# Kernel optimization log

Measured on AMD Instinct MI355X. Metric: run time of the kernel, lower is better.

The kernel has to match this reference:

```python
import jax, jax.numpy as jnp
import numpy as np

TEMPERATURE = 1.0


def setup_inputs() -> dict:
    key = jax.random.key(0)
    k1, k2, k3 = jax.random.split(key, 3)
    B, N, D = 4, 4096, 128
    x = jax.random.normal(k1, (B, N, D), dtype=jnp.float32)
    # nn.Linear(dim, dim): weight [D, D], bias [D] (kaiming-uniform-ish scale)
    bound = 1.0 / np.sqrt(D)
    W = jax.random.uniform(k2, (D, D), dtype=jnp.float32, minval=-bound, maxval=bound)
    b = jax.random.uniform(k3, (D,), dtype=jnp.float32, minval=-bound, maxval=bound)
    return {"x": x, "W": W, "b": b}


def reference(x, W, b):
    # Linear projection (torch Linear: x @ W.T + b)
    h = jnp.einsum('bnd,ed->bne', x, W) + b            # [B, N, D]
    # Pairwise Euclidean distance via ||a||^2 + ||b||^2 - 2 a.b (avoids O(N^2*D) diff tensor)
    sq = jnp.sum(h * h, axis=-1)                        # [B, N]
    gram = jnp.einsum('bnd,bmd->bnm', h, h)             # [B, N, N]
    d2 = jnp.maximum(sq[:, :, None] + sq[:, None, :] - 2.0 * gram, 0.0)
    distances = jnp.sqrt(d2)                            # [B, N, N]
    return jnp.exp(-distances * TEMPERATURE)
```

## Files before the change

kernel.cpp:

```cpp
#include <hip/hip_runtime.h>


typedef float  f32x4   __attribute__((ext_vector_type(4)));
typedef float  f32x16  __attribute__((ext_vector_type(16)));
typedef short  bf16x8  __attribute__((ext_vector_type(8)));
typedef __attribute__((address_space(3))) void       lds_void_t;
typedef const __attribute__((address_space(1))) void gvoid_t;

__device__ inline float bf2f(unsigned int u) {
    union { unsigned int i; float f; } c; c.i = u << 16; return c.f;
}
__device__ inline unsigned short f2bf(float f) {
    union { float f; unsigned int i; } c; c.f = f;
    unsigned int r = c.i + 0x7fffu + ((c.i >> 16) & 1u);
    return (unsigned short)(r >> 16);
}

#define KA_ROWS 32
__global__ __launch_bounds__(256) void proj_kernel(
    const float* __restrict__ x, const float* __restrict__ W,
    const float* __restrict__ bias, unsigned short* __restrict__ h,
    float* __restrict__ sq)
{
    __shared__ __align__(16) unsigned short W5[32 * 4 * 32 * 4];
    __shared__ float xs[KA_ROWS][132];
    const int t = threadIdx.x;
    const long r0 = (long)blockIdx.x * KA_ROWS;

    for (int q = t; q < 4096; q += 256) {
        float4 w4 = ((const float4*)W)[q];
        int e = q >> 5, d4 = q & 31;
        int eb = e >> 2, ei = e & 3;
        ushort4 o;
        o.x = f2bf(w4.x); o.y = f2bf(w4.y); o.z = f2bf(w4.z); o.w = f2bf(w4.w);
        *(ushort4*)&W5[d4 * 256 + ei * 64 + ((eb ^ d4) & 31) * 4] = o;
    }
    const float4* xsrc = (const float4*)(x + r0 * 128);
    for (int q = t; q < KA_ROWS * 32; q += 256) {
        float4 v = xsrc[q];
        int r = q >> 5, d = (q & 31) << 2;
        xs[r][d] = v.x; xs[r][d + 1] = v.y; xs[r][d + 2] = v.z; xs[r][d + 3] = v.w;
    }
    __syncthreads();

    const int eb = t & 31, rb = t >> 5;
    const int e0 = eb * 4, rr0 = rb * 4;

    float acc_[4][4];
    #pragma unroll
    for (int ei = 0; ei < 4; ++ei) {
        float bv = bias[e0 + ei];
        #pragma unroll
        for (int ri = 0; ri < 4; ++ri) acc_[ri][ei] = bv;
    }

    for (int d4 = 0; d4 < 32; ++d4) {
        float wv[4][4];
        #pragma unroll
        for (int ei = 0; ei < 4; ++ei) {
            ushort4 u = *(const ushort4*)&W5[d4 * 256 + ei * 64 + ((eb ^ d4) & 31) * 4];
            wv[ei][0] = bf2f(u.x); wv[ei][1] = bf2f(u.y);
            wv[ei][2] = bf2f(u.z); wv[ei][3] = bf2f(u.w);
        }
        #pragma unroll
        for (int ri = 0; ri < 4; ++ri) {
            float4 xv = *(const float4*)&xs[rr0 + ri][d4 * 4];
            #pragma unroll
            for (int ei = 0; ei < 4; ++ei) {
                acc_[ri][ei] = fmaf(xv.x, wv[ei][0],
                               fmaf(xv.y, wv[ei][1],
                               fmaf(xv.z, wv[ei][2],
                               fmaf(xv.w, wv[ei][3], acc_[ri][ei]))));
            }
        }
    }

    float s[4] = {0.f, 0.f, 0.f, 0.f};
    #pragma unroll
    for (int ri = 0; ri < 4; ++ri) {
        ushort4 o;
        float v0 = bf2f(o.x = f2bf(acc_[ri][0]));
        float v1 = bf2f(o.y = f2bf(acc_[ri][1]));
        float v2 = bf2f(o.z = f2bf(acc_[ri][2]));
        float v3 = bf2f(o.w = f2bf(acc_[ri][3]));
        s[ri] = v0 * v0 + v1 * v1 + v2 * v2 + v3 * v3;
        *(ushort4*)&h[(r0 + rr0 + ri) * 128 + e0] = o;
    }
    #pragma unroll
    for (int ri = 0; ri < 4; ++ri) {
        #pragma unroll
        for (int m = 16; m > 0; m >>= 1) s[ri] += __shfl_xor(s[ri], m, 64);
    }
    if (eb == 0) {
        #pragma unroll
        for (int ri = 0; ri < 4; ++ri) sq[r0 + rr0 + ri] = s[ri];
    }
}

__global__ __launch_bounds__(512, 2) void gram_kernel(
    const unsigned short* __restrict__ h, const float* __restrict__ sq,
    float* __restrict__ out)
{
    __shared__ __align__(16) unsigned short hsI[256 * 128];
    __shared__ __align__(16) unsigned short hsJ[256 * 128];
    const int bid = blockIdx.x;
    const int xcd = bid & 7;
    const int bb  = xcd >> 1;
    const int tloc = ((bid >> 3) << 1) | (xcd & 1);
    const int it = tloc >> 4, jt = tloc & 15;
    const int i0 = bb * 4096 + it * 256;
    const int j0 = bb * 4096 + jt * 256;
    const int t = threadIdx.x, w = t >> 6, lane = t & 63;

    const char* hb = (const char*)h;
    #pragma unroll
    for (int q = 0; q < 8; ++q) {
        int p   = (q * 512 + t) << 4;
        int row = p >> 8;
        int c   = (p >> 4) & 15;
        int cs  = c ^ (row & 15);
        unsigned off = (unsigned)p;
        __builtin_amdgcn_global_load_lds(
            (gvoid_t*)(hb + ((long)(i0 + row) << 8) + (cs << 4)),
            (lds_void_t*)(((char*)hsI) + off), 16, 0, 0);
        __builtin_amdgcn_global_load_lds(
            (gvoid_t*)(hb + ((long)(j0 + row) << 8) + (cs << 4)),
            (lds_void_t*)(((char*)hsJ) + off), 16, 0, 0);
    }
    __syncthreads();

    const int wr = w >> 2, wc = w & 3;
    const int l31 = lane & 31, lh = lane >> 5;
    f32x16 acc[4][2] = {};
    const char* hI = (const char*)hsI;
    const char* hJ = (const char*)hsJ;

    #pragma unroll
    for (int ks = 0; ks < 8; ++ks) {
        bf16x8 af[4], bg[2];
        #pragma unroll
        for (int rb = 0; rb < 4; ++rb) {
            int rowA = wr * 128 + rb * 32 + l31;
            int cA = ((ks * 2 + lh) ^ (rowA & 15)) << 4;
            af[rb] = *(const bf16x8*)(hI + (rowA << 8) + cA);
        }
        #pragma unroll
        for (int nb = 0; nb < 2; ++nb) {
            int rowB = wc * 64 + nb * 32 + l31;
            int cB = ((ks * 2 + lh) ^ (rowB & 15)) << 4;
            bg[nb] = *(const bf16x8*)(hJ + (rowB << 8) + cB);
        }
        #pragma unroll
        for (int rb = 0; rb < 4; ++rb)
            #pragma unroll
            for (int nb = 0; nb < 2; ++nb)
                acc[rb][nb] = __builtin_amdgcn_mfma_f32_32x32x16_bf16(
                    af[rb], bg[nb], acc[rb][nb], 0, 0, 0);
    }

    float sqj_r[2];
    #pragma unroll
    for (int nb = 0; nb < 2; ++nb) sqj_r[nb] = sq[j0 + wc * 64 + nb * 32 + l31];

    #pragma unroll
    for (int rb = 0; rb < 4; ++rb) {
        #pragma unroll
        for (int reg = 0; reg < 16; ++reg) {
            int il = wr * 128 + rb * 32 + (reg & 3) + 8 * (reg >> 2) + 4 * lh;
            float sqi_v = sq[i0 + il];
            #pragma unroll
            for (int nb = 0; nb < 2; ++nb) {
                int jl = wc * 64 + nb * 32 + l31;
                float g  = acc[rb][nb][reg];
                float d2 = fmaxf(fmaf(g, -2.0f, sqi_v + sqj_r[nb]), 0.0f);
                float val = __expf(-sqrtf(d2));
                if (it == jt && il == jl) val = 1.0f;
                __builtin_nontemporal_store(
                    val, &out[((long)(i0 + il) << 12) + (jt << 8) + jl]);
            }
        }
    }
}

extern "C" void kernel_launch(void* const* d_in, const int* in_sizes, int n_in,
                              void* d_out, int out_size, void* d_ws, size_t ws_size,
                              hipStream_t stream) {
    const float* x = (const float*)d_in[0];
    const float* W = (const float*)d_in[1];
    const float* b = (const float*)d_in[2];
    float* out = (float*)d_out;

    unsigned short* h = (unsigned short*)d_ws;
    float* sq = (float*)((char*)d_ws + (size_t)16384 * 128 * 2);

    proj_kernel<<<dim3(16384 / KA_ROWS), dim3(256), 0, stream>>>(x, W, b, h, sq);
    gram_kernel<<<dim3(1024), dim3(512), 0, stream>>>(h, sq, out);
}
```

Measured before the change: 82.97 us.

## Restructure gram kernel: A fragments in registers, stream j-tiles, halve LDS

Each wave now keeps its 32 rows of the I tile in registers, loaded straight from global memory, so the I tile no longer goes through LDS and only the J tile is staged. The loop walks over eight 32-column J subtiles, computing one accumulator at a time and storing results right away. This is meant to cut LDS usage and accumulator registers so four blocks can be resident per CU instead of two, overlapping epilogue stores with MFMA work. The cost is fewer MFMAs per B-fragment LDS read, lowering reuse of each load.

```diff
diff --git a/kernel.cpp b/kernel.cpp
--- a/kernel.cpp
+++ b/kernel.cpp
@@ -97,12 +97,12 @@
     }
 }
 
-__global__ __launch_bounds__(512, 2) void gram_kernel(
+__global__ __launch_bounds__(512, 4) void gram_kernel(
     const unsigned short* __restrict__ h, const float* __restrict__ sq,
     float* __restrict__ out)
 {
-    __shared__ __align__(16) unsigned short hsI[256 * 128];
     __shared__ __align__(16) unsigned short hsJ[256 * 128];
+    __shared__ float sqj_s[256];
     const int bid = blockIdx.x;
     const int xcd = bid & 7;
     const int bb  = xcd >> 1;
@@ -111,73 +111,69 @@
     const int i0 = bb * 4096 + it * 256;
     const int j0 = bb * 4096 + jt * 256;
     const int t = threadIdx.x, w = t >> 6, lane = t & 63;
+    const int l31 = lane & 31, lh = lane >> 5;
+    const char* hb = (const char*)h;
 
-    const char* hb = (const char*)h;
     #pragma unroll
     for (int q = 0; q < 8; ++q) {
         int p   = (q * 512 + t) << 4;
         int row = p >> 8;
         int c   = (p >> 4) & 15;
         int cs  = c ^ (row & 15);
-        unsigned off = (unsigned)p;
-        __builtin_amdgcn_global_load_lds(
-            (gvoid_t*)(hb + ((long)(i0 + row) << 8) + (cs << 4)),
-            (lds_void_t*)(((char*)hsI) + off), 16, 0, 0);
         __builtin_amdgcn_global_load_lds(
             (gvoid_t*)(hb + ((long)(j0 + row) << 8) + (cs << 4)),
-            (lds_void_t*)(((char*)hsJ) + off), 16, 0, 0);
+            (lds_void_t*)(((char*)hsJ) + (unsigned)p), 16, 0, 0);
     }
+    if (t < 256) sqj_s[t] = sq[j0 + t];
+
+    bf16x8 af[8];
+    {
+        const char* base = hb + ((long)(i0 + w * 32 + l31) << 8);
+        #pragma unroll
+        for (int ks = 0; ks < 8; ++ks)
+            af[ks] = *(const bf16x8*)(base + ((ks * 2 + lh) << 4));
+    }
+    float sqi_r[16];
+    #pragma unroll
+    for (int reg = 0; reg < 16; ++reg)
+        sqi_r[reg] = sq[i0 + w * 32 + (reg & 3) + 8 * (reg >> 2) + 4 * lh];
+
+    float* ob = out + ((size_t)bb << 24) + ((size_t)(it * 256) << 12) + jt * 256;
+    unsigned voff[16];
+    #pragma unroll
+    for (int reg = 0; reg < 16; ++reg) {
+        int il = w * 32 + (reg & 3) + 8 * (reg >> 2) + 4 * lh;
+        voff[reg] = ((unsigned)il << 12) + l31;
+    }
+
     __syncthreads();
-
-    const int wr = w >> 2, wc = w & 3;
-    const int l31 = lane & 31, lh = lane >> 5;
-    f32x16 acc[4][2] = {};
-    const char* hI = (const char*)hsI;
     const char* hJ = (const char*)hsJ;
+    const bool diag = (it == jt);
 
     #pragma unroll
-    for (int ks = 0; ks < 8; ++ks) {
-        bf16x8 af[4], bg[2];
+    for (int js = 0; js < 8; ++js) {
+        const int rowB = js * 32 + l31;
+        bf16x8 bg[8];
         #pragma unroll
-        for (int rb = 0; rb < 4; ++rb) {
-            int rowA = wr * 128 + rb * 32 + l31;
-            int cA = ((ks * 2 + lh) ^ (rowA & 15)) << 4;
-            af[rb] = *(const bf16x8*)(hI + (rowA << 8) + cA);
+        for (int ks = 0; ks < 8; ++ks) {
+            int cB = ((ks * 2 + lh) ^ (rowB & 15)) << 4;
+            bg[ks] = *(const bf16x8*)(hJ + (rowB << 8) + cB);
         }
+        f32x16 acc = {};
         #pragma unroll
-        for (int nb = 0; nb < 2; ++nb) {
-            int rowB = wc * 64 + nb * 32 + l31;
-            int cB = ((ks * 2 + lh) ^ (rowB & 15)) << 4;
-            bg[nb] = *(const bf16x8*)(hJ + (rowB << 8) + cB);
-        }
-        #pragma unroll
-        for (int rb = 0; rb < 4; ++rb)
-            #pragma unroll
-            for (int nb = 0; nb < 2; ++nb)
-                acc[rb][nb] = __builtin_amdgcn_mfma_f32_32x32x16_bf16(
-                    af[rb], bg[nb], acc[rb][nb], 0, 0, 0);
-    }
+        for (int ks = 0; ks < 8; ++ks)
+            acc = __builtin_amdgcn_mfma_f32_32x32x16_bf16(af[ks], bg[ks], acc, 0, 0, 0);
 
-    float sqj_r[2];
-    #pragma unroll
-    for (int nb = 0; nb < 2; ++nb) sqj_r[nb] = sq[j0 + wc * 64 + nb * 32 + l31];
-
-    #pragma unroll
-    for (int rb = 0; rb < 4; ++rb) {
+        const float sqj = sqj_s[rowB];
         #pragma unroll
         for (int reg = 0; reg < 16; ++reg) {
-            int il = wr * 128 + rb * 32 + (reg & 3) + 8 * (reg >> 2) + 4 * lh;
-            float sqi_v = sq[i0 + il];
-            #pragma unroll
-            for (int nb = 0; nb < 2; ++nb) {
-                int jl = wc * 64 + nb * 32 + l31;
-                float g  = acc[rb][nb][reg];
-                float d2 = fmaxf(fmaf(g, -2.0f, sqi_v + sqj_r[nb]), 0.0f);
-                float val = __expf(-sqrtf(d2));
-                if (it == jt && il == jl) val = 1.0f;
-                __builtin_nontemporal_store(
-                    val, &out[((long)(i0 + il) << 12) + (jt << 8) + jl]);
+            float d2 = fmaxf(fmaf(acc[reg], -2.0f, sqi_r[reg] + sqj), 0.0f);
+            float val = __expf(-sqrtf(d2));
+            if (diag && w == js) {
+                int rl = (reg & 3) + 8 * (reg >> 2) + 4 * lh;
+                if (rl == l31) val = 1.0f;
             }
+            __builtin_nontemporal_store(val, ob + voff[reg] + js * 32);
         }
     }
 }
```

Measured after the change: 126.2 us. 1.52x slower.

## Stage gram output tiles through LDS for coalesced 16-byte stores

Applied to the files above, without the earlier changes.

The epilogue now writes the computed exp values back into the accumulator registers, then stages each 128x256 half-tile in the shared-memory buffer once the operand tiles are no longer needed. It then stores whole rows with 16-byte vectorized nontemporal writes, replacing scattered 4-byte stores. It also swaps sqrtf for the raw hardware sqrt builtin. The aim is to make the write-bound output stream fully coalesced, at the cost of extra LDS traffic and barriers.

```diff
diff --git a/kernel.cpp b/kernel.cpp
--- a/kernel.cpp
+++ b/kernel.cpp
@@ -101,8 +101,11 @@
     const unsigned short* __restrict__ h, const float* __restrict__ sq,
     float* __restrict__ out)
 {
-    __shared__ __align__(16) unsigned short hsI[256 * 128];
-    __shared__ __align__(16) unsigned short hsJ[256 * 128];
+    __shared__ __align__(16) char smem[131072];
+    unsigned short* hsI = (unsigned short*)smem;
+    unsigned short* hsJ = (unsigned short*)(smem + 65536);
+    float* stg = (float*)smem;
+
     const int bid = blockIdx.x;
     const int xcd = bid & 7;
     const int bb  = xcd >> 1;
@@ -119,13 +122,12 @@
         int row = p >> 8;
         int c   = (p >> 4) & 15;
         int cs  = c ^ (row & 15);
-        unsigned off = (unsigned)p;
         __builtin_amdgcn_global_load_lds(
             (gvoid_t*)(hb + ((long)(i0 + row) << 8) + (cs << 4)),
-            (lds_void_t*)(((char*)hsI) + off), 16, 0, 0);
+            (lds_void_t*)(((char*)hsI) + (unsigned)p), 16, 0, 0);
         __builtin_amdgcn_global_load_lds(
             (gvoid_t*)(hb + ((long)(j0 + row) << 8) + (cs << 4)),
-            (lds_void_t*)(((char*)hsJ) + off), 16, 0, 0);
+            (lds_void_t*)(((char*)hsJ) + (unsigned)p), 16, 0, 0);
     }
     __syncthreads();
 
@@ -171,14 +173,44 @@
             #pragma unroll
             for (int nb = 0; nb < 2; ++nb) {
                 int jl = wc * 64 + nb * 32 + l31;
-                float g  = acc[rb][nb][reg];
-                float d2 = fmaxf(fmaf(g, -2.0f, sqi_v + sqj_r[nb]), 0.0f);
-                float val = __expf(-sqrtf(d2));
+                float d2 = fmaxf(fmaf(acc[rb][nb][reg], -2.0f, sqi_v + sqj_r[nb]), 0.0f);
+                float val = __expf(-__builtin_amdgcn_sqrtf(d2));
                 if (it == jt && il == jl) val = 1.0f;
-                __builtin_nontemporal_store(
-                    val, &out[((long)(i0 + il) << 12) + (jt << 8) + jl]);
+                acc[rb][nb][reg] = val;
             }
         }
+    }
+
+    float* ob = out + ((long)i0 << 12) + (jt << 8);
+
+    asm volatile("s_waitcnt lgkmcnt(0)" ::: "memory");
+    __builtin_amdgcn_s_barrier();
+
+    #pragma unroll
+    for (int hh = 0; hh < 2; ++hh) {
+        if (wr == hh) {
+            #pragma unroll
+            for (int rb = 0; rb < 4; ++rb)
+                #pragma unroll
+                for (int reg = 0; reg < 16; ++reg) {
+                    int row = rb * 32 + (reg & 3) + 8 * (reg >> 2) + 4 * lh;
+                    #pragma unroll
+                    for (int nb = 0; nb < 2; ++nb)
+                        stg[row * 256 + wc * 64 + nb * 32 + l31] = acc[rb][nb][reg];
+                }
+        }
+        asm volatile("s_waitcnt lgkmcnt(0)" ::: "memory");
+        __builtin_amdgcn_s_barrier();
+
+        #pragma unroll
+        for (int k = 0; k < 16; ++k) {
+            int r = w * 16 + k;
+            f32x4 v = *(const f32x4*)&stg[r * 256 + (lane << 2)];
+            __builtin_nontemporal_store(
+                v, (f32x4*)(ob + ((long)(hh * 128 + r) << 12) + (lane << 2)));
+        }
+        asm volatile("s_waitcnt lgkmcnt(0)" ::: "memory");
+        __builtin_amdgcn_s_barrier();
     }
 }
 
```

Result: slower. 88.07 us (+6.1%).
